# Kernel tuning notes

Hardware: AMD Instinct MI355X
Metric: run time of the kernel (lower is better)

## Reference

```python
import jax, jax.numpy as jnp
import numpy as np

B, L, T = 8192, 1024, 4  # batch, seq_len, n_tags (BMES)


def setup_inputs() -> dict:
    key = jax.random.key(0)
    k1, k2, k3, k4, k5 = jax.random.split(key, 5)
    return {
        "s_tag": jax.random.normal(k1, (B, L, T), dtype=jnp.float32),
        "tags": jax.random.randint(k2, (B, L), 0, T),
        "mask": jnp.ones((B, L), dtype=bool),
        "trans_score": (jax.random.normal(k3, (T, T), dtype=jnp.float32) * 0.1),
        "start_score": (jax.random.normal(k4, (T,), dtype=jnp.float32) * 0.1),
        "end_score": (jax.random.normal(k5, (T,), dtype=jnp.float32) * 0.1),
    }


def reference(s_tag, tags, mask, trans_score, start_score, end_score):
    # forward() path of LinearCRFWordSegmentation: loss = (logZ - gold_score)/B.
    # Note: forward calls set_mask(False), so the structural masks are unused.
    b, l, t = s_tag.shape
    bidx = jnp.arange(b)
    end_pos = mask.sum(axis=-1) - 1  # [B] index of last valid position

    # ---- gold path score (get_scores) ----
    emit = jnp.take_along_axis(s_tag, tags[..., None], axis=-1)[..., 0]  # [B,L]
    trans = trans_score[tags[:, :-1], tags[:, 1:]]                        # [B,L-1]
    per_pos = emit + jnp.pad(trans, ((0, 0), (1, 0)))                     # [B,L]
    score = jnp.sum(jnp.where(mask, per_pos, jnp.float32(0)))
    score = score + start_score[tags[:, 0]].sum()
    score = score + end_score[tags[bidx, end_pos]].sum()

    # ---- log partition (crf): sequential logsumexp recurrence over tags ----
    s0 = s_tag[:, 0] + start_score  # [B,T]

    def step(s_prev, emit_t):
        # [B,T_prev,1] + [1,T_prev,T_cur] + [B,1,T_cur] -> logsumexp over prev
        s_new = jax.nn.logsumexp(
            s_prev[:, :, None] + trans_score[None] + emit_t[:, None, :], axis=1
        )
        return s_new, s_new

    emits = jnp.swapaxes(s_tag, 0, 1)  # [L,B,T]
    _, ss = jax.lax.scan(step, s0, emits[1:])      # [L-1,B,T]
    ss = jnp.concatenate([s0[None], ss], axis=0)    # [L,B,T] alpha trellis
    final = ss[end_pos, bidx] + end_score           # [B,T]
    logZ = jax.nn.logsumexp(final, axis=-1).sum()

    return (logZ - score) / jnp.float32(b)
```

## Files before the change

### kernel.cpp

```cpp
#include <hip/hip_runtime.h>

#define Bn 8192
#define Ln 1024
#define NBLOCK (Bn / 2)

#define LOG2E 1.4426950408889634f
#define LN2f  0.6931471805599453f

typedef float f32x2 __attribute__((ext_vector_type(2)));

__device__ __forceinline__ float sel4(float4 v, int t) {
    float r = v.x;
    r = (t == 1) ? v.y : r;
    r = (t == 2) ? v.z : r;
    r = (t == 3) ? v.w : r;
    return r;
}

__device__ __forceinline__ float rfl(float x) {
    return __int_as_float(__builtin_amdgcn_readfirstlane(__float_as_int(x)));
}

__device__ __forceinline__ float fexp2(float x) {
    float r;
    asm("v_exp_f32 %0, %1" : "=v"(r) : "v"(x));
    return r;
}

__device__ __forceinline__ f32x2 pkmax(f32x2 a, f32x2 b) {
    return (f32x2){fmaxf(a.x, b.x), fmaxf(a.y, b.y)};
}

template <int LEVELS>
__device__ __forceinline__ void butterfly(float p[4][4], int& scale, int lane) {
#pragma unroll
    for (int s = 0; s < LEVELS; s++) {
        const int m = 1 << s;
        float q[4][4];
#pragma unroll
        for (int i = 0; i < 4; i++)
#pragma unroll
            for (int j = 0; j < 4; j++) q[i][j] = __shfl_xor(p[i][j], m);
        int sc2 = __shfl_xor(scale, m);
        bool upper = (lane & m) != 0;

        float acc[4][4];
#pragma unroll
        for (int i = 0; i < 4; i++)
#pragma unroll
            for (int j = 0; j < 4; j++) acc[i][j] = 0.f;
#pragma unroll
        for (int k = 0; k < 4; k++) {
#pragma unroll
            for (int i = 0; i < 4; i++) {
                float a = upper ? q[i][k] : p[i][k];
#pragma unroll
                for (int j = 0; j < 4; j++) {
                    float bv = upper ? p[k][j] : q[k][j];
                    acc[i][j] = fmaf(a, bv, acc[i][j]);
                }
            }
        }
#pragma unroll
        for (int i = 0; i < 4; i++)
#pragma unroll
            for (int j = 0; j < 4; j++) p[i][j] = acc[i][j];
        scale += sc2;

        float mx = p[0][0];
#pragma unroll
        for (int i = 0; i < 4; i++)
#pragma unroll
            for (int j = 0; j < 4; j++) mx = fmaxf(mx, p[i][j]);
        unsigned eb = (__float_as_uint(mx) >> 23) & 0xffu;
        scale += (int)eb - 126;
        float ms = __uint_as_float((unsigned)(253 - eb) << 23);
#pragma unroll
        for (int i = 0; i < 4; i++)
#pragma unroll
            for (int j = 0; j < 4; j++) p[i][j] *= ms;
    }
}

__global__ __launch_bounds__(256) void crf_all(
    const float* __restrict__ s_tag, const int* __restrict__ tags,
    const float* __restrict__ trans, const float* __restrict__ start_s,
    const float* __restrict__ end_s, float* __restrict__ diffs)
{
    __shared__ float4 sS[2048];

    const int wv = threadIdx.x >> 6;
    const int lw = threadIdx.x & 63;
    const int hb = (blockIdx.x << 2) | wv;

    const float4* __restrict__ srow = (const float4*)s_tag + (size_t)hb * 512;
    const int*    __restrict__ trow = tags + (size_t)hb * 512;
    float4* slice = &sS[wv * 512];

    int prev_c = trow[(hb & 1) ? -1 : 0];

    const int4* trow4 = (const int4*)trow;
    int4 ta = trow4[2 * lw], tb = trow4[2 * lw + 1];

    const int swl = lw ^ ((lw >> 3) & 7);
    float4 v[8];
#pragma unroll
    for (int k = 0; k < 8; k++) v[k] = srow[64 * k + swl];

    unsigned tgp = (unsigned)(ta.x & 3) | ((unsigned)(ta.y & 3) << 2)
                 | ((unsigned)(ta.z & 3) << 4) | ((unsigned)(ta.w & 3) << 6)
                 | ((unsigned)(tb.x & 3) << 8) | ((unsigned)(tb.y & 3) << 10)
                 | ((unsigned)(tb.z & 3) << 12) | ((unsigned)(tb.w & 3) << 14);
    const bool skip0 = ((hb & 1) == 0) && (lw == 0);

    int pl = (int)((__shfl((int)tgp, (lw + 63) & 63) >> 14) & 3);
    int prev = (lw == 0) ? (prev_c & 3) : pl;

    float vtr = trans[lw & 15];
    float trsum = 0.f;
    {
        int pt = prev;
#pragma unroll
        for (int j = 0; j < 8; j++) {
            int tj = (int)((tgp >> (2 * j)) & 3);
            float g = __shfl(vtr, pt * 4 + tj);
            trsum += (skip0 && j == 0) ? 0.f : g;
            pt = tj;
        }
    }
    float es[4][4];
#pragma unroll
    for (int k = 0; k < 4; k++)
#pragma unroll
        for (int j = 0; j < 4; j++)
            es[k][j] = rfl(fexp2(trans[k * 4 + j] * LOG2E));

#pragma unroll
    for (int k = 0; k < 8; k++) slice[64 * k + lw] = v[k];

    f32x2 pc[4][2];
#pragma unroll
    for (int j = 0; j < 4; j++) {
        pc[j][0] = (f32x2){(j == 0) ? 1.f : 0.f, (j == 1) ? 1.f : 0.f};
        pc[j][1] = (f32x2){(j == 2) ? 1.f : 0.f, (j == 3) ? 1.f : 0.f};
    }
    int scale = 0;
    float emitsum = 0.f;

#pragma unroll
    for (int j = 0; j < 8; j++) {
        float4 stj = slice[8 * lw + (j ^ (lw & 7))];
        int tj = (int)((tgp >> (2 * j)) & 3);
        emitsum += sel4(stj, tj);
        if (!(skip0 && j == 0)) {
            float f0 = fexp2(stj.x * LOG2E);
            float f1 = fexp2(stj.y * LOG2E);
            float f2 = fexp2(stj.z * LOG2E);
            float f3 = fexp2(stj.w * LOG2E);

            f32x2 n00 = pc[0][0] * es[0][0] + pc[1][0] * es[1][0] + pc[2][0] * es[2][0] + pc[3][0] * es[3][0];
            f32x2 n01 = pc[0][1] * es[0][0] + pc[1][1] * es[1][0] + pc[2][1] * es[2][0] + pc[3][1] * es[3][0];
            f32x2 n10 = pc[0][0] * es[0][1] + pc[1][0] * es[1][1] + pc[2][0] * es[2][1] + pc[3][0] * es[3][1];
            f32x2 n11 = pc[0][1] * es[0][1] + pc[1][1] * es[1][1] + pc[2][1] * es[2][1] + pc[3][1] * es[3][1];
            f32x2 n20 = pc[0][0] * es[0][2] + pc[1][0] * es[1][2] + pc[2][0] * es[2][2] + pc[3][0] * es[3][2];
            f32x2 n21 = pc[0][1] * es[0][2] + pc[1][1] * es[1][2] + pc[2][1] * es[2][2] + pc[3][1] * es[3][2];
            f32x2 n30 = pc[0][0] * es[0][3] + pc[1][0] * es[1][3] + pc[2][0] * es[2][3] + pc[3][0] * es[3][3];
            f32x2 n31 = pc[0][1] * es[0][3] + pc[1][1] * es[1][3] + pc[2][1] * es[2][3] + pc[3][1] * es[3][3];
            pc[0][0] = n00 * f0; pc[0][1] = n01 * f0;
            pc[1][0] = n10 * f1; pc[1][1] = n11 * f1;
            pc[2][0] = n20 * f2; pc[2][1] = n21 * f2;
            pc[3][0] = n30 * f3; pc[3][1] = n31 * f3;
        }
    }
    {
        f32x2 mm = pkmax(pkmax(pkmax(pc[0][0], pc[0][1]), pkmax(pc[1][0], pc[1][1])),
                         pkmax(pkmax(pc[2][0], pc[2][1]), pkmax(pc[3][0], pc[3][1])));
        float mx = fmaxf(mm.x, mm.y);
        unsigned eb = (__float_as_uint(mx) >> 23) & 0xffu;
        scale += (int)eb - 126;
        float ms = __uint_as_float((unsigned)(253 - eb) << 23);
#pragma unroll
        for (int jj = 0; jj < 4; jj++) { pc[jj][0] *= ms; pc[jj][1] *= ms; }
    }

    float p[4][4];
#pragma unroll
    for (int i = 0; i < 4; i++)
#pragma unroll
        for (int j = 0; j < 4; j++) p[i][j] = pc[j][i >> 1][i & 1];

    butterfly<3>(p, scale, lw);

    float sc = emitsum + trsum;
#pragma unroll
    for (int m = 1; m < 64; m <<= 1) sc += __shfl_xor(sc, m);

    __syncthreads();

    float4* exM = sS;
    int*    exK = (int*)(sS + 128);
    float*  exS = (float*)(sS + 136);

    if ((lw & 7) == 0) {
        int m = wv * 8 + (lw >> 3);
        exM[m * 4 + 0] = make_float4(p[0][0], p[0][1], p[0][2], p[0][3]);
        exM[m * 4 + 1] = make_float4(p[1][0], p[1][1], p[1][2], p[1][3]);
        exM[m * 4 + 2] = make_float4(p[2][0], p[2][1], p[2][2], p[2][3]);
        exM[m * 4 + 3] = make_float4(p[3][0], p[3][1], p[3][2], p[3][3]);
        exK[m] = scale;
    }
    if (lw == 0) exS[wv] = sc;
    __syncthreads();

    if (threadIdx.x < 32) {
        const int t   = threadIdx.x;
        const int sub = t & 15;
        const int bl  = t >> 4;
        const long long batch = 2LL * blockIdx.x + bl;

        float4 r0 = exM[(bl * 16 + sub) * 4 + 0];
        float4 r1 = exM[(bl * 16 + sub) * 4 + 1];
        float4 r2 = exM[(bl * 16 + sub) * 4 + 2];
        float4 r3 = exM[(bl * 16 + sub) * 4 + 3];
        float pf[4][4] = {{r0.x, r0.y, r0.z, r0.w}, {r1.x, r1.y, r1.z, r1.w},
                          {r2.x, r2.y, r2.z, r2.w}, {r3.x, r3.y, r3.z, r3.w}};
        int fsc = exK[bl * 16 + sub];

        butterfly<4>(pf, fsc, sub);

        if (sub == 0) {
            float4 st0 = *((const float4*)s_tag + (size_t)batch * Ln);
            float a0 = exp2f((st0.x + start_s[0]) * LOG2E);
            float a1 = exp2f((st0.y + start_s[1]) * LOG2E);
            float a2 = exp2f((st0.z + start_s[2]) * LOG2E);
            float a3 = exp2f((st0.w + start_s[3]) * LOG2E);

            float n0 = a0 * pf[0][0] + a1 * pf[1][0] + a2 * pf[2][0] + a3 * pf[3][0];
            float n1 = a0 * pf[0][1] + a1 * pf[1][1] + a2 * pf[2][1] + a3 * pf[3][1];
            float n2 = a0 * pf[0][2] + a1 * pf[1][2] + a2 * pf[2][2] + a3 * pf[3][2];
            float n3 = a0 * pf[0][3] + a1 * pf[1][3] + a2 * pf[2][3] + a3 * pf[3][3];

            float sfin = n0 * exp2f(end_s[0] * LOG2E) + n1 * exp2f(end_s[1] * LOG2E)
                       + n2 * exp2f(end_s[2] * LOG2E) + n3 * exp2f(end_s[3] * LOG2E);
            float logZ = (log2f(sfin) + (float)fsc) * LN2f;

            int t0 = tags[(size_t)batch * Ln];
            int tE = tags[(size_t)batch * Ln + Ln - 1];
            float gold = exS[2 * bl] + exS[2 * bl + 1] + start_s[t0] + end_s[tE];
            diffs[batch] = logZ - gold;
        }
    }
}

__global__ __launch_bounds__(1024) void crf_pass3(
    const float* __restrict__ diffs, float* __restrict__ out)
{
    __shared__ float sm[1024];
    float s = 0.f;
    for (int i = threadIdx.x; i < Bn; i += 1024) s += diffs[i];
    sm[threadIdx.x] = s;
    __syncthreads();
    for (int off = 512; off > 0; off >>= 1) {
        if ((int)threadIdx.x < off) sm[threadIdx.x] += sm[threadIdx.x + off];
        __syncthreads();
    }
    if (threadIdx.x == 0) out[0] = sm[0] / (float)Bn;
}

extern "C" void kernel_launch(void* const* d_in, const int* in_sizes, int n_in,
                              void* d_out, int out_size, void* d_ws, size_t ws_size,
                              hipStream_t stream)
{
    const float* s_tag  = (const float*)d_in[0];
    const int*   tags   = (const int*)d_in[1];
    const float* trans  = (const float*)d_in[3];
    const float* starts = (const float*)d_in[4];
    const float* ends   = (const float*)d_in[5];

    float* diffs = (float*)d_ws;

    crf_all<<<dim3(NBLOCK), dim3(256), 0, stream>>>(
        s_tag, tags, trans, starts, ends, diffs);
    crf_pass3<<<dim3(1), dim3(1024), 0, stream>>>(diffs, (float*)d_out);
}
```

Before: 48.60 us.

## Load emissions directly per lane, drop LDS staging, one batch per block

Each lane now loads its eight contiguous float4 emissions straight from global memory into registers, so the LDS transpose through a 32KB shared buffer is no longer needed. Blocks shrink to 128 threads handling one batch row, which doubles the grid and frees LDS for higher occupancy. The final reduction kernel now reads diffs with float4 loads. The trade-off is that each lane's global loads are strided rather than coalesced across the wavefront.

```diff
diff --git a/kernel.cpp b/kernel.cpp
--- a/kernel.cpp
+++ b/kernel.cpp
@@ -2,7 +2,7 @@
 
 #define Bn 8192
 #define Ln 1024
-#define NBLOCK (Bn / 2)
+#define NBLOCK Bn
 
 #define LOG2E 1.4426950408889634f
 #define LN2f  0.6931471805599453f
@@ -82,36 +82,40 @@
     }
 }
 
-__global__ __launch_bounds__(256) void crf_all(
+__global__ __launch_bounds__(128) void crf_all(
     const float* __restrict__ s_tag, const int* __restrict__ tags,
     const float* __restrict__ trans, const float* __restrict__ start_s,
     const float* __restrict__ end_s, float* __restrict__ diffs)
 {
-    __shared__ float4 sS[2048];
+    __shared__ float4 exM[64];
+    __shared__ int    exK[16];
+    __shared__ float  exS[2];
 
     const int wv = threadIdx.x >> 6;
     const int lw = threadIdx.x & 63;
-    const int hb = (blockIdx.x << 2) | wv;
-
-    const float4* __restrict__ srow = (const float4*)s_tag + (size_t)hb * 512;
-    const int*    __restrict__ trow = tags + (size_t)hb * 512;
-    float4* slice = &sS[wv * 512];
-
-    int prev_c = trow[(hb & 1) ? -1 : 0];
+    const long long batch = blockIdx.x;
+    const size_t hb = ((size_t)batch << 1) | (unsigned)wv;
+
+    const float4* __restrict__ srow = (const float4*)s_tag + hb * 512;
+    const int*    __restrict__ trow = tags + hb * 512;
+
+    int prev_c = trow[wv ? -1 : 0];
 
     const int4* trow4 = (const int4*)trow;
     int4 ta = trow4[2 * lw], tb = trow4[2 * lw + 1];
 
-    const int swl = lw ^ ((lw >> 3) & 7);
-    float4 v[8];
-#pragma unroll
-    for (int k = 0; k < 8; k++) v[k] = srow[64 * k + swl];
+    const float4* lane_ptr = srow + 8 * lw;
+    float4 va[4], vb[4];
+#pragma unroll
+    for (int k = 0; k < 4; k++) va[k] = lane_ptr[k];
+#pragma unroll
+    for (int k = 0; k < 4; k++) vb[k] = lane_ptr[k + 4];
 
     unsigned tgp = (unsigned)(ta.x & 3) | ((unsigned)(ta.y & 3) << 2)
                  | ((unsigned)(ta.z & 3) << 4) | ((unsigned)(ta.w & 3) << 6)
                  | ((unsigned)(tb.x & 3) << 8) | ((unsigned)(tb.y & 3) << 10)
                  | ((unsigned)(tb.z & 3) << 12) | ((unsigned)(tb.w & 3) << 14);
-    const bool skip0 = ((hb & 1) == 0) && (lw == 0);
+    const bool skip0 = (wv == 0) && (lw == 0);
 
     int pl = (int)((__shfl((int)tgp, (lw + 63) & 63) >> 14) & 3);
     int prev = (lw == 0) ? (prev_c & 3) : pl;
@@ -135,9 +139,6 @@
         for (int j = 0; j < 4; j++)
             es[k][j] = rfl(fexp2(trans[k * 4 + j] * LOG2E));
 
-#pragma unroll
-    for (int k = 0; k < 8; k++) slice[64 * k + lw] = v[k];
-
     f32x2 pc[4][2];
 #pragma unroll
     for (int j = 0; j < 4; j++) {
@@ -149,7 +150,7 @@
 
 #pragma unroll
     for (int j = 0; j < 8; j++) {
-        float4 stj = slice[8 * lw + (j ^ (lw & 7))];
+        float4 stj = (j < 4) ? va[j & 3] : vb[j & 3];
         int tj = (int)((tgp >> (2 * j)) & 3);
         emitsum += sel4(stj, tj);
         if (!(skip0 && j == 0)) {
@@ -195,12 +196,6 @@
 #pragma unroll
     for (int m = 1; m < 64; m <<= 1) sc += __shfl_xor(sc, m);
 
-    __syncthreads();
-
-    float4* exM = sS;
-    int*    exK = (int*)(sS + 128);
-    float*  exS = (float*)(sS + 136);
-
     if ((lw & 7) == 0) {
         int m = wv * 8 + (lw >> 3);
         exM[m * 4 + 0] = make_float4(p[0][0], p[0][1], p[0][2], p[0][3]);
@@ -212,19 +207,16 @@
     if (lw == 0) exS[wv] = sc;
     __syncthreads();
 
-    if (threadIdx.x < 32) {
-        const int t   = threadIdx.x;
-        const int sub = t & 15;
-        const int bl  = t >> 4;
-        const long long batch = 2LL * blockIdx.x + bl;
-
-        float4 r0 = exM[(bl * 16 + sub) * 4 + 0];
-        float4 r1 = exM[(bl * 16 + sub) * 4 + 1];
-        float4 r2 = exM[(bl * 16 + sub) * 4 + 2];
-        float4 r3 = exM[(bl * 16 + sub) * 4 + 3];
+    if (threadIdx.x < 16) {
+        const int sub = threadIdx.x;
+
+        float4 r0 = exM[sub * 4 + 0];
+        float4 r1 = exM[sub * 4 + 1];
+        float4 r2 = exM[sub * 4 + 2];
+        float4 r3 = exM[sub * 4 + 3];
         float pf[4][4] = {{r0.x, r0.y, r0.z, r0.w}, {r1.x, r1.y, r1.z, r1.w},
                           {r2.x, r2.y, r2.z, r2.w}, {r3.x, r3.y, r3.z, r3.w}};
-        int fsc = exK[bl * 16 + sub];
+        int fsc = exK[sub];
 
         butterfly<4>(pf, fsc, sub);
 
@@ -246,7 +238,7 @@
 
             int t0 = tags[(size_t)batch * Ln];
             int tE = tags[(size_t)batch * Ln + Ln - 1];
-            float gold = exS[2 * bl] + exS[2 * bl + 1] + start_s[t0] + end_s[tE];
+            float gold = exS[0] + exS[1] + start_s[t0] + end_s[tE];
             diffs[batch] = logZ - gold;
         }
     }
@@ -256,9 +248,10 @@
     const float* __restrict__ diffs, float* __restrict__ out)
 {
     __shared__ float sm[1024];
-    float s = 0.f;
-    for (int i = threadIdx.x; i < Bn; i += 1024) s += diffs[i];
-    sm[threadIdx.x] = s;
+    const float4* d4 = (const float4*)diffs;
+    float4 a = d4[threadIdx.x];
+    float4 b = d4[threadIdx.x + 1024];
+    sm[threadIdx.x] = (a.x + a.y) + (a.z + a.w) + (b.x + b.y) + (b.z + b.w);
     __syncthreads();
     for (int off = 512; off > 0; off >>= 1) {
         if ((int)threadIdx.x < off) sm[threadIdx.x] += sm[threadIdx.x + off];
@@ -279,7 +272,7 @@
 
     float* diffs = (float*)d_ws;
 
-    crf_all<<<dim3(NBLOCK), dim3(256), 0, stream>>>(
+    crf_all<<<dim3(NBLOCK), dim3(128), 0, stream>>>(
         s_tag, tags, trans, starts, ends, diffs);
     crf_pass3<<<dim3(1), dim3(1024), 0, stream>>>(diffs, (float*)d_out);
 }
```

Measured after the change: 50.42 us. 3.8% more time.
